# Kernel optimization log

Measured on AMD Instinct MI355X. Metric: run time of the kernel, lower is better.

The kernel has to match this reference:

```python
import jax, jax.numpy as jnp
import numpy as np
from jax.scipy.special import gammaln

N, E, IN, HID, OUT, K, BESSEL_TERMS = 50000, 800000, 64, 64, 32, 10, 20


def setup_inputs() -> dict:
    key = jax.random.key(0)
    ks = jax.random.split(key, 6)
    x = jax.random.normal(ks[0], (N, IN), dtype=jnp.float32)
    edge_index = jax.random.randint(ks[1], (2, E), 0, N, dtype=jnp.int32)
    theta_direct = jax.random.normal(ks[2], (IN, HID), dtype=jnp.float32)
    theta_heat1 = jax.random.normal(ks[3], (IN, HID), dtype=jnp.float32)
    theta_hidden = jax.random.normal(ks[4], (HID, OUT), dtype=jnp.float32)
    theta_heat2 = jax.random.normal(ks[5], (HID, OUT), dtype=jnp.float32)
    t = jnp.array(0.1, dtype=jnp.float32)
    return dict(x=x, edge_index=edge_index, theta_direct=theta_direct,
                theta_heat1=theta_heat1, theta_hidden=theta_hidden,
                theta_heat2=theta_heat2, t=t)


def _bessel_iv(orders, t):
    # Modified Bessel I_v(t) via power series; differentiable in t (t>0, small).
    m = jnp.arange(BESSEL_TERMS, dtype=jnp.float32)  # [M]
    v = orders[:, None]                              # [K,1]
    log_terms = (2.0 * m + v) * jnp.log(t * 0.5) - gammaln(m + 1.0) - gammaln(m + v + 1.0)
    return jnp.exp(log_terms).sum(-1)                # [K]


def _heat_kernel(x, row, col, w, coeffs):
    # Chebyshev recurrence on tilde_L = L_sym - I = -(D^-1/2 A D^-1/2)
    def spmm(v):
        return -jax.ops.segment_sum(w[:, None] * v[col], row, num_segments=N)
    out = coeffs[0] * x
    Tkm2, Tkm1 = x, spmm(x)
    out = out + coeffs[1] * Tkm1
    for k in range(2, K):
        Tk = 2.0 * spmm(Tkm1) - Tkm2
        out = out + coeffs[k] * Tk
        Tkm2, Tkm1 = Tkm1, Tk
    return out


def reference(x, edge_index, theta_direct, theta_heat1, theta_hidden, theta_heat2, t):
    row, col = edge_index[0], edge_index[1]
    # sym-normalized Laplacian edge weights (PyG get_laplacian semantics)
    deg = jax.ops.segment_sum(jnp.ones(E, x.dtype), row, num_segments=N)
    dinv = jnp.where(deg > 0, deg ** -0.5, 0.0)
    w = dinv[row] * dinv[col]                         # [E]
    orders = jnp.arange(K, dtype=jnp.float32)
    iv = _bessel_iv(orders, t)                        # [K]
    signs = jnp.where(orders % 2 == 0, 2.0, -2.0)
    coeffs = (signs * iv).at[0].set(iv[0])            # c0=I0(t), ck=2(-1)^k I_k(t)
    x_heat = _heat_kernel(x, row, col, w, coeffs)
    hidden = jax.nn.relu(x @ theta_direct + x_heat @ theta_heat1)
    hidden_heat = _heat_kernel(hidden, row, col, w, coeffs)
    out = hidden @ theta_hidden + hidden_heat @ theta_heat2
    return jax.nn.log_softmax(out, axis=1)
```

## Files before the change

kernel.cpp:

```cpp
#include <hip/hip_runtime.h>
#include <math.h>

#define N 50000
#define E 800000
#define KCHEB 10
#define BT 20
#define N64 ((size_t)N * 64)
#define UROW ((size_t)(N + 1) * 64)
#define CONV_BLOCKS 1563
#define XU_BLOCKS 1563
#define PAD_BLOCKS 196
#define NB 196
#define EPB 2048
#define ABLK ((E + EPB - 1) / EPB)
#define BCAP 5120
#define PHASE_GRID 1024
#define NGROUP 3125

typedef __attribute__((ext_vector_type(8))) short short8;
typedef __attribute__((ext_vector_type(4))) float f32x4;

__device__ __forceinline__ unsigned f2bf(float x) {
    unsigned u = __float_as_uint(x);
    return (u + 0x7FFFu + ((u >> 16) & 1u)) >> 16;
}
__device__ __forceinline__ float bf2f(unsigned h) {
    return __uint_as_float(h << 16);
}
__device__ __forceinline__ unsigned packbf(float lo, float hi) {
    return f2bf(lo) | (f2bf(hi) << 16);
}
__device__ __forceinline__ void unpack8(uint4 v, float* f) {
    f[0]=bf2f(v.x&0xFFFFu); f[1]=bf2f(v.x>>16);
    f[2]=bf2f(v.y&0xFFFFu); f[3]=bf2f(v.y>>16);
    f[4]=bf2f(v.z&0xFFFFu); f[5]=bf2f(v.z>>16);
    f[6]=bf2f(v.w&0xFFFFu); f[7]=bf2f(v.w>>16);
}
__device__ __forceinline__ uint4 pack8(const float* f) {
    return make_uint4(packbf(f[0],f[1]),packbf(f[2],f[3]),packbf(f[4],f[5]),packbf(f[6],f[7]));
}

__device__ __forceinline__ void pack_one(const float* Wtop, const float* Wbot,
                                         int ncols, uint4* out, int id) {
    int ntiles = ncols >> 4;
    int lane = id & 63;
    int nt = (id >> 6) % ntiles;
    int kt = id / (64 * ntiles);
    int n = nt * 16 + (lane & 15);
    int k0 = kt * 32 + (lane >> 4) * 8;
    const float* src = (k0 < 64) ? (Wtop + k0 * ncols + n) : (Wbot + (k0 - 64) * ncols + n);
    unsigned r[4];
#pragma unroll
    for (int p = 0; p < 4; p++)
        r[p] = packbf(src[(2 * p) * ncols], src[(2 * p + 1) * ncols]);
    out[id] = make_uint4(r[0], r[1], r[2], r[3]);
}

__global__ __launch_bounds__(256) void k1_bucket_conv_pack(
        const int* __restrict__ row, const int* __restrict__ col,
        int* __restrict__ btail, int2* __restrict__ bucketArr,
        const float4* __restrict__ xin, uint4* __restrict__ xbf,
        const float* __restrict__ Wd, const float* __restrict__ Wh1,
        const float* __restrict__ Whd, const float* __restrict__ Wh2,
        uint4* __restrict__ Wfrag1, uint4* __restrict__ Wfrag2) {
    int b = blockIdx.x, tid = threadIdx.x;
    if (b < ABLK) {
        __shared__ int2 buf[EPB];
        __shared__ int cnt[256];
        __shared__ int offs[256];
        __shared__ int gb[256];
        int base = b * EPB;
        int n = E - base; if (n > EPB) n = EPB;
        int r[8], c[8], p[8];
        cnt[tid] = 0;
        __syncthreads();
#pragma unroll
        for (int j = 0; j < 8; j++) {
            int e = base + j * 256 + tid;
            if (e < base + n) {
                r[j] = row[e]; c[j] = col[e];
                p[j] = atomicAdd(&cnt[r[j] >> 8], 1);
            } else r[j] = -1;
        }
        __syncthreads();
        offs[tid] = cnt[tid];
        __syncthreads();
        for (int o = 1; o < 256; o <<= 1) {
            int u = (tid >= o) ? offs[tid - o] : 0;
            __syncthreads();
            offs[tid] += u;
            __syncthreads();
        }
        int excl = offs[tid] - cnt[tid];
        __syncthreads();
        offs[tid] = excl;
        if (tid < NB && cnt[tid] > 0) gb[tid] = atomicAdd(&btail[tid], cnt[tid]);
        __syncthreads();
#pragma unroll
        for (int j = 0; j < 8; j++)
            if (r[j] >= 0) buf[offs[r[j] >> 8] + p[j]] = make_int2(r[j], c[j]);
        __syncthreads();
        for (int i = tid; i < n; i += 256) {
            int2 eg = buf[i];
            int bb = eg.x >> 8;
            int pos = gb[bb] + (i - offs[bb]);
            if (pos < BCAP) bucketArr[(size_t)bb * BCAP + pos] = eg;
        }
    } else if (b < ABLK + CONV_BLOCKS) {
        int i = (b - ABLK) * 256 + tid;
        if (i < (int)(N64 / 8)) {
            float4 a = xin[2 * i], c = xin[2 * i + 1];
            uint4 o;
            o.x = packbf(a.x, a.y); o.y = packbf(a.z, a.w);
            o.z = packbf(c.x, c.y); o.w = packbf(c.z, c.w);
            xbf[i] = o;
        }
    } else if (b < ABLK + CONV_BLOCKS + 4) {
        int id = (b - ABLK - CONV_BLOCKS) * 256 + tid;
        if (id < 1024) pack_one(Wd, Wh1, 64, Wfrag1, id);
    } else {
        int id = (b - ABLK - CONV_BLOCKS - 4) * 256 + tid;
        if (id < 512) pack_one(Whd, Wh2, 32, Wfrag2, id);
    }
}

__global__ __launch_bounds__(256) void k_ell(
        const int2* __restrict__ bucketArr, const int* __restrict__ btail,
        int* __restrict__ ell, int* __restrict__ deg) {
    __shared__ int rcnt[256];
    int b = blockIdx.x, tid = threadIdx.x;
    rcnt[tid] = 0;
    __syncthreads();
    int cnt = btail[b]; if (cnt > BCAP) cnt = BCAP;
    const int2* src = bucketArr + (size_t)b * BCAP;
    for (int i = tid; i < cnt; i += 256) {
        int2 eg = src[i];
        int s = atomicAdd(&rcnt[eg.x & 255], 1);
        if (s < 64) ell[(size_t)eg.x * 64 + s] = eg.y << 7;
    }
    __syncthreads();
    int rr = (b << 8) + tid;
    if (rr < N) deg[rr] = rcnt[tid];
}

__global__ __launch_bounds__(256) void k2_node(
        const float* __restrict__ x, const int* __restrict__ deg,
        float* __restrict__ dinv, unsigned short* __restrict__ xu,
        int* __restrict__ ell, unsigned short* __restrict__ Uarr,
        unsigned short* __restrict__ hidu, int nslots,
        const float* __restrict__ tptr, float* __restrict__ coeffs,
        int* __restrict__ kmaxp) {
    __shared__ float sc[KCHEB];
    int b = blockIdx.x, tid = threadIdx.x;
    if (b < XU_BLOCKS) {
        int i = b * 256 + tid;
        if (i < (int)(N64 / 8)) {
            int r = i >> 3, sub = i & 7;
            int d = deg[r];
            float dr = (d > 0) ? rsqrtf((float)d) : 0.f;
            const float* xp = x + (size_t)r * 64 + sub * 8;
            float4 a = *(const float4*)xp, c = *(const float4*)(xp + 4);
            float f[8] = {dr*a.x, dr*a.y, dr*a.z, dr*a.w, dr*c.x, dr*c.y, dr*c.z, dr*c.w};
            ((uint4*)xu)[i] = pack8(f);
            if (sub == 0) dinv[r] = dr;
        } else if (i < (int)(N64 / 8) + 8) {
            ((uint4*)xu)[i] = make_uint4(0, 0, 0, 0);
        }
    } else if (b < XU_BLOCKS + PAD_BLOCKS) {
        int r = (b - XU_BLOCKS) * 256 + tid;
        if (r < N) {
            int d = deg[r]; if (d > 64) d = 64;
            int dpad = (d + 7) & ~7;
            for (int j = d; j < dpad; j++) ell[(size_t)r * 64 + j] = (N << 7);
        }
    } else if (b == XU_BLOCKS + PAD_BLOCKS) {
        int total = (nslots + 1) * 8;
        if (tid < total) {
            int which = tid >> 3, q = tid & 7;
            uint4* dst = (which < nslots)
                ? (uint4*)(Uarr + (size_t)which * UROW + (size_t)N * 64)
                : (uint4*)(hidu + (size_t)N * 64);
            dst[q] = make_uint4(0, 0, 0, 0);
        }
    } else {
        int v = tid;
        if (v < KCHEB) {
            float tt = tptr[0];
            float lt = logf(0.5f * tt);
            float s = 0.f;
            for (int m = 0; m < BT; m++) {
                float lg = lgammaf((float)m + 1.0f) + lgammaf((float)(m + v) + 1.0f);
                s += expf((2.0f * m + (float)v) * lt - lg);
            }
            float c;
            if (v == 0) c = s;
            else c = ((v & 1) == 0) ? 2.0f * s : -2.0f * s;
            coeffs[v] = c;
            sc[v] = c;
        }
        __syncthreads();
        if (v == 0) {
            float c0 = fabsf(sc[0]);
            int kmax = 1;
            for (int k = 1; k < KCHEB; k++)
                if (fabsf(sc[k]) >= 0.00390625f * c0) kmax = k;
            kmaxp[0] = kmax;
        }
    }
}

__global__ __launch_bounds__(256, 4) void spmm_phase(
        const int* __restrict__ deg, const int* __restrict__ ell,
        const unsigned short* __restrict__ baseu, const unsigned short* __restrict__ baseT,
        unsigned short* __restrict__ Tarr, unsigned short* __restrict__ Uarr,
        int nslots, const float* __restrict__ dinv,
        const int* __restrict__ kmaxp, int* __restrict__ barcnt) {
    int tid = threadIdx.x;
    int lane = tid & 63;
    int lane8 = lane & 7;
    int gbase = lane & 56;
    int h = (lane >> 3) & 1;
    int myoff16 = lane8 * 16;
    int kmax = kmaxp[0]; if (kmax > KCHEB - 1) kmax = KCHEB - 1;
    for (int k = 1; k <= kmax; k++) {
        const unsigned short* uin = (k == 1) ? baseu
                                  : Uarr + (size_t)((k - 2) % nslots) * UROW;
        const uint4* tkm2 = (const uint4*)((k <= 2) ? baseT
                                  : Tarr + (size_t)((k - 3) % nslots) * N64);
        uint4* Tout = (uint4*)(Tarr + (size_t)((k - 1) % nslots) * N64);
        uint4* Uout = (uint4*)(Uarr + (size_t)((k - 1) % nslots) * UROW);
        const char* vbase = (const char*)uin;
        for (int rb = blockIdx.x; rb < NGROUP; rb += PHASE_GRID) {
            int r = rb * 16 + (tid >> 6) * 4 + (lane >> 4);
            int d = deg[r]; if (d > 64) d = 64;
            int dpad = (d + 7) & ~7;
            const int* erow = ell + (size_t)r * 64;
            float a0=0,a1=0,a2=0,a3=0,a4=0,a5=0,a6=0,a7=0;
            for (int j0 = h * 8; j0 < dpad; j0 += 16) {
                int myoff = erow[j0 + lane8];
#pragma unroll
                for (int i = 0; i < 8; i++) {
                    int off = __shfl(myoff, gbase + i, 64);
                    uint4 v = *(const uint4*)(vbase + off + myoff16);
                    a0 += bf2f(v.x & 0xFFFFu);
                    a1 += bf2f(v.x >> 16);
                    a2 += bf2f(v.y & 0xFFFFu);
                    a3 += bf2f(v.y >> 16);
                    a4 += bf2f(v.z & 0xFFFFu);
                    a5 += bf2f(v.z >> 16);
                    a6 += bf2f(v.w & 0xFFFFu);
                    a7 += bf2f(v.w >> 16);
                }
            }
            a0 += __shfl_xor(a0, 8, 64);
            a1 += __shfl_xor(a1, 8, 64);
            a2 += __shfl_xor(a2, 8, 64);
            a3 += __shfl_xor(a3, 8, 64);
            a4 += __shfl_xor(a4, 8, 64);
            a5 += __shfl_xor(a5, 8, 64);
            a6 += __shfl_xor(a6, 8, 64);
            a7 += __shfl_xor(a7, 8, 64);
            if (h == 0) {
                float dr = dinv[r];
                float ndr = -dr;
                float s0=ndr*a0, s1=ndr*a1, s2=ndr*a2, s3=ndr*a3;
                float s4=ndr*a4, s5=ndr*a5, s6=ndr*a6, s7=ndr*a7;
                int idx = r * 8 + lane8;
                if (k >= 2) {
                    uint4 tm = tkm2[idx];
                    s0 = 2.f*s0 - bf2f(tm.x & 0xFFFFu);
                    s1 = 2.f*s1 - bf2f(tm.x >> 16);
                    s2 = 2.f*s2 - bf2f(tm.y & 0xFFFFu);
                    s3 = 2.f*s3 - bf2f(tm.y >> 16);
                    s4 = 2.f*s4 - bf2f(tm.z & 0xFFFFu);
                    s5 = 2.f*s5 - bf2f(tm.z >> 16);
                    s6 = 2.f*s6 - bf2f(tm.w & 0xFFFFu);
                    s7 = 2.f*s7 - bf2f(tm.w >> 16);
                }
                float t8[8] = {s0,s1,s2,s3,s4,s5,s6,s7};
                Tout[idx] = pack8(t8);
                float u8[8] = {dr*s0,dr*s1,dr*s2,dr*s3,dr*s4,dr*s5,dr*s6,dr*s7};
                Uout[idx] = pack8(u8);
            }
        }
        if (k < kmax) {
            __threadfence();
            __syncthreads();
            if (tid == 0) {
                __hip_atomic_fetch_add(barcnt, 1, __ATOMIC_ACQ_REL, __HIP_MEMORY_SCOPE_AGENT);
                int target = PHASE_GRID * k;
                while (__hip_atomic_load(barcnt, __ATOMIC_ACQUIRE, __HIP_MEMORY_SCOPE_AGENT) < target)
                    __builtin_amdgcn_s_sleep(8);
            }
            __syncthreads();
        }
    }
}

__global__ __launch_bounds__(256) void matmul_hidden(
        const unsigned short* __restrict__ basebf, const unsigned short* __restrict__ Tarr,
        int nslots, const float* __restrict__ coeffs, const int* __restrict__ kmaxp,
        const uint4* __restrict__ Wfrag, unsigned short* __restrict__ hidbf,
        const float* __restrict__ dinv, unsigned short* __restrict__ hidu) {
    __shared__ __align__(16) unsigned short At[64][136];
    int tid = threadIdx.x;
    int row0 = blockIdx.x * 64;
    int kmax = kmaxp[0]; if (kmax > KCHEB - 1) kmax = KCHEB - 1;
    float c0 = coeffs[0];
    for (int u = tid; u < 1024; u += 256) {
        int rr = u >> 4, seg = u & 15;
        int r = row0 + rr;
        uint4 val = make_uint4(0, 0, 0, 0);
        int col;
        if (seg < 8) {
            col = seg * 8;
            if (r < N) val = *(const uint4*)(basebf + (size_t)r * 64 + seg * 8);
        } else {
            int s = seg - 8;
            col = 64 + s * 8;
            if (r < N) {
                uint4 xv = *(const uint4*)(basebf + (size_t)r * 64 + s * 8);
                float h[8], f[8];
                unpack8(xv, f);
#pragma unroll
                for (int q = 0; q < 8; q++) h[q] = c0 * f[q];
                for (int j = 1; j <= kmax; j++) {
                    const unsigned short* Tj = Tarr + (size_t)((j - 1) % nslots) * N64;
                    uint4 tv = *(const uint4*)(Tj + (size_t)r * 64 + s * 8);
                    float g[8];
                    unpack8(tv, g);
                    float cj = coeffs[j];
#pragma unroll
                    for (int q = 0; q < 8; q++) h[q] = fmaf(cj, g[q], h[q]);
                }
                val = pack8(h);
            }
        }
        *(uint4*)&At[rr][col] = val;
    }
    __syncthreads();
    int wv = tid >> 6, lane = tid & 63;
    int m0 = wv * 16;
    short8 afr[4];
#pragma unroll
    for (int kt = 0; kt < 4; kt++)
        afr[kt] = *(const short8*)&At[m0 + (lane & 15)][kt * 32 + (lane >> 4) * 8];
    f32x4 acc[4];
#pragma unroll
    for (int nt = 0; nt < 4; nt++) acc[nt] = (f32x4){0.f, 0.f, 0.f, 0.f};
#pragma unroll
    for (int nt = 0; nt < 4; nt++) {
#pragma unroll
        for (int kt = 0; kt < 4; kt++) {
            short8 bfr = *(const short8*)&Wfrag[kt * 256 + nt * 64 + lane];
            acc[nt] = __builtin_amdgcn_mfma_f32_16x16x32_bf16(afr[kt], bfr, acc[nt], 0, 0, 0);
        }
    }
    float drow[4];
#pragma unroll
    for (int i = 0; i < 4; i++) {
        int r = row0 + m0 + (lane >> 4) * 4 + i;
        drow[i] = (r < N) ? dinv[r] : 0.f;
    }
#pragma unroll
    for (int nt = 0; nt < 4; nt++) {
#pragma unroll
        for (int i = 0; i < 4; i++) {
            int r = row0 + m0 + (lane >> 4) * 4 + i;
            if (r < N) {
                float hv = fmaxf(acc[nt][i], 0.f);
                size_t o = (size_t)r * 64 + nt * 16 + (lane & 15);
                hidbf[o] = (unsigned short)f2bf(hv);
                hidu[o]  = (unsigned short)f2bf(drow[i] * hv);
            }
        }
    }
}

__global__ __launch_bounds__(256) void matmul_out(
        const unsigned short* __restrict__ basebf, const unsigned short* __restrict__ Tarr,
        int nslots, const float* __restrict__ coeffs, const int* __restrict__ kmaxp,
        const uint4* __restrict__ Wfrag, float* __restrict__ out) {
    __shared__ __align__(16) unsigned short At[64][136];
    int tid = threadIdx.x;
    int row0 = blockIdx.x * 64;
    int kmax = kmaxp[0]; if (kmax > KCHEB - 1) kmax = KCHEB - 1;
    float c0 = coeffs[0];
    for (int u = tid; u < 1024; u += 256) {
        int rr = u >> 4, seg = u & 15;
        int r = row0 + rr;
        uint4 val = make_uint4(0, 0, 0, 0);
        int col;
        if (seg < 8) {
            col = seg * 8;
            if (r < N) val = *(const uint4*)(basebf + (size_t)r * 64 + seg * 8);
        } else {
            int s = seg - 8;
            col = 64 + s * 8;
            if (r < N) {
                uint4 xv = *(const uint4*)(basebf + (size_t)r * 64 + s * 8);
                float h[8], f[8];
                unpack8(xv, f);
#pragma unroll
                for (int q = 0; q < 8; q++) h[q] = c0 * f[q];
                for (int j = 1; j <= kmax; j++) {
                    const unsigned short* Tj = Tarr + (size_t)((j - 1) % nslots) * N64;
                    uint4 tv = *(const uint4*)(Tj + (size_t)r * 64 + s * 8);
                    float g[8];
                    unpack8(tv, g);
                    float cj = coeffs[j];
#pragma unroll
                    for (int q = 0; q < 8; q++) h[q] = fmaf(cj, g[q], h[q]);
                }
                val = pack8(h);
            }
        }
        *(uint4*)&At[rr][col] = val;
    }
    __syncthreads();
    int wv = tid >> 6, lane = tid & 63;
    int m0 = wv * 16;
    short8 afr[4];
#pragma unroll
    for (int kt = 0; kt < 4; kt++)
        afr[kt] = *(const short8*)&At[m0 + (lane & 15)][kt * 32 + (lane >> 4) * 8];
    f32x4 acc[2];
    acc[0] = (f32x4){0.f, 0.f, 0.f, 0.f};
    acc[1] = (f32x4){0.f, 0.f, 0.f, 0.f};
#pragma unroll
    for (int nt = 0; nt < 2; nt++) {
#pragma unroll
        for (int kt = 0; kt < 4; kt++) {
            short8 bfr = *(const short8*)&Wfrag[kt * 128 + nt * 64 + lane];
            acc[nt] = __builtin_amdgcn_mfma_f32_16x16x32_bf16(afr[kt], bfr, acc[nt], 0, 0, 0);
        }
    }
#pragma unroll
    for (int i = 0; i < 4; i++) {
        float f0 = acc[0][i], f1 = acc[1][i];
        float m = fmaxf(f0, f1);
#pragma unroll
        for (int o = 1; o < 16; o <<= 1) m = fmaxf(m, __shfl_xor(m, o, 64));
        float s = expf(f0 - m) + expf(f1 - m);
#pragma unroll
        for (int o = 1; o < 16; o <<= 1) s += __shfl_xor(s, o, 64);
        float ls = m + logf(s);
        int r = row0 + m0 + (lane >> 4) * 4 + i;
        if (r < N) {
            out[(size_t)r * 32 + (lane & 15)] = f0 - ls;
            out[(size_t)r * 32 + 16 + (lane & 15)] = f1 - ls;
        }
    }
}

extern "C" void kernel_launch(void* const* d_in, const int* in_sizes, int n_in,
                              void* d_out, int out_size, void* d_ws, size_t ws_size,
                              hipStream_t stream) {
    const float* x   = (const float*)d_in[0];
    const int*   ei  = (const int*)d_in[1];
    const float* Wd  = (const float*)d_in[2];
    const float* Wh1 = (const float*)d_in[3];
    const float* Whd = (const float*)d_in[4];
    const float* Wh2 = (const float*)d_in[5];
    const float* tp  = (const float*)d_in[6];
    const int* row = ei;
    const int* col = ei + E;

    size_t off = 0;
    auto alloc = [&](size_t bytes) -> void* {
        void* p = (char*)d_ws + off;
        off += (bytes + 255) & ~(size_t)255;
        return p;
    };
    int*   btail  = (int*)alloc((size_t)512 * 4);
    int*   bar1   = btail + 256;
    int*   bar2   = btail + 257;
    int*   deg    = (int*)alloc((size_t)N * 4);
    float* dinv   = (float*)alloc((size_t)N * 4);
    float* coeffs = (float*)alloc(KCHEB * 4);
    int*   kmaxp  = (int*)alloc(4);
    int*   ell    = (int*)alloc((size_t)N * 64 * 4);
    int2*  bucketArr = (int2*)alloc((size_t)NB * BCAP * 8);
    unsigned short* xbf   = (unsigned short*)alloc(N64 * 2);
    unsigned short* xu    = (unsigned short*)alloc(UROW * 2);
    unsigned short* hidbf = (unsigned short*)alloc(N64 * 2);
    unsigned short* hidu  = (unsigned short*)alloc(UROW * 2);
    uint4* Wfrag1 = (uint4*)alloc(1024 * 16);
    uint4* Wfrag2 = (uint4*)alloc(512 * 16);
    size_t per_slot = N64 * 2 + UROW * 2 + 512;
    int nslots = (int)((ws_size - off) / per_slot);
    if (nslots > KCHEB - 1) nslots = KCHEB - 1;
    if (nslots < 3) nslots = 3;
    unsigned short* Tarr = (unsigned short*)alloc((size_t)nslots * N64 * 2);
    unsigned short* Uarr = (unsigned short*)alloc((size_t)nslots * UROW * 2);

    hipMemsetAsync(btail, 0, (size_t)512 * 4, stream);

    k1_bucket_conv_pack<<<ABLK + CONV_BLOCKS + 6, 256, 0, stream>>>(
        row, col, btail, bucketArr, (const float4*)x, (uint4*)xbf,
        Wd, Wh1, Whd, Wh2, Wfrag1, Wfrag2);
    k_ell<<<NB, 256, 0, stream>>>(bucketArr, btail, ell, deg);
    k2_node<<<XU_BLOCKS + PAD_BLOCKS + 2, 256, 0, stream>>>(
        x, deg, dinv, xu, ell, Uarr, hidu, nslots, tp, coeffs, kmaxp);

    const int mm_grid = (N + 63) / 64;

    spmm_phase<<<PHASE_GRID, 256, 0, stream>>>(deg, ell, xu, xbf,
                                               Tarr, Uarr, nslots, dinv, kmaxp, bar1);
    matmul_hidden<<<mm_grid, 256, 0, stream>>>(xbf, Tarr, nslots, coeffs, kmaxp,
                                               Wfrag1, hidbf, dinv, hidu);

    spmm_phase<<<PHASE_GRID, 256, 0, stream>>>(deg, ell, hidu, hidbf,
                                               Tarr, Uarr, nslots, dinv, kmaxp, bar2);
    matmul_out<<<mm_grid, 256, 0, stream>>>(hidbf, Tarr, nslots, coeffs, kmaxp,
                                            Wfrag2, (float*)d_out);
}
```

Measured before the change: 171.6 us.

## Fuse ELL build with node scaling and raise spmm phase grid and occupancy

Merges the ELL construction kernel and the node preprocessing kernel into one launch. Each bucket block now computes degree, dinv, padding and the dinv-scaled bf16 copy of x for its own 256 rows, and the coefficient block also zeroes the sentinel rows. Separately, the persistent spmm phase grid is doubled and the launch bounds are raised to 8 blocks per CU. The fusion removes one launch and a round trip of deg through memory, but the xu conversion now runs on only 196 blocks. The higher occupancy target may also cause register spills.

Measured after the change: 233.0 us. 1.36x slower.

```diff
diff --git a/kernel.cpp b/kernel.cpp
--- a/kernel.cpp
+++ b/kernel.cpp
@@ -8,13 +8,11 @@
 #define N64 ((size_t)N * 64)
 #define UROW ((size_t)(N + 1) * 64)
 #define CONV_BLOCKS 1563
-#define XU_BLOCKS 1563
-#define PAD_BLOCKS 196
 #define NB 196
 #define EPB 2048
 #define ABLK ((E + EPB - 1) / EPB)
 #define BCAP 5120
-#define PHASE_GRID 1024
+#define PHASE_GRID 2048
 #define NGROUP 3125
 
 typedef __attribute__((ext_vector_type(8))) short short8;
@@ -124,65 +122,55 @@
     }
 }
 
-__global__ __launch_bounds__(256) void k_ell(
+__global__ __launch_bounds__(256) void k_ell_fused(
         const int2* __restrict__ bucketArr, const int* __restrict__ btail,
-        int* __restrict__ ell, int* __restrict__ deg) {
-    __shared__ int rcnt[256];
-    int b = blockIdx.x, tid = threadIdx.x;
-    rcnt[tid] = 0;
-    __syncthreads();
-    int cnt = btail[b]; if (cnt > BCAP) cnt = BCAP;
-    const int2* src = bucketArr + (size_t)b * BCAP;
-    for (int i = tid; i < cnt; i += 256) {
-        int2 eg = src[i];
-        int s = atomicAdd(&rcnt[eg.x & 255], 1);
-        if (s < 64) ell[(size_t)eg.x * 64 + s] = eg.y << 7;
-    }
-    __syncthreads();
-    int rr = (b << 8) + tid;
-    if (rr < N) deg[rr] = rcnt[tid];
-}
-
-__global__ __launch_bounds__(256) void k2_node(
-        const float* __restrict__ x, const int* __restrict__ deg,
-        float* __restrict__ dinv, unsigned short* __restrict__ xu,
-        int* __restrict__ ell, unsigned short* __restrict__ Uarr,
+        int* __restrict__ ell, int* __restrict__ deg,
+        const float* __restrict__ x, float* __restrict__ dinv,
+        unsigned short* __restrict__ xu, unsigned short* __restrict__ Uarr,
         unsigned short* __restrict__ hidu, int nslots,
         const float* __restrict__ tptr, float* __restrict__ coeffs,
         int* __restrict__ kmaxp) {
-    __shared__ float sc[KCHEB];
     int b = blockIdx.x, tid = threadIdx.x;
-    if (b < XU_BLOCKS) {
-        int i = b * 256 + tid;
-        if (i < (int)(N64 / 8)) {
-            int r = i >> 3, sub = i & 7;
-            int d = deg[r];
-            float dr = (d > 0) ? rsqrtf((float)d) : 0.f;
-            const float* xp = x + (size_t)r * 64 + sub * 8;
-            float4 a = *(const float4*)xp, c = *(const float4*)(xp + 4);
-            float f[8] = {dr*a.x, dr*a.y, dr*a.z, dr*a.w, dr*c.x, dr*c.y, dr*c.z, dr*c.w};
-            ((uint4*)xu)[i] = pack8(f);
-            if (sub == 0) dinv[r] = dr;
-        } else if (i < (int)(N64 / 8) + 8) {
-            ((uint4*)xu)[i] = make_uint4(0, 0, 0, 0);
-        }
-    } else if (b < XU_BLOCKS + PAD_BLOCKS) {
-        int r = (b - XU_BLOCKS) * 256 + tid;
-        if (r < N) {
-            int d = deg[r]; if (d > 64) d = 64;
+    if (b < NB) {
+        __shared__ int rcnt[256];
+        __shared__ float sdr[256];
+        rcnt[tid] = 0;
+        __syncthreads();
+        int cnt = btail[b]; if (cnt > BCAP) cnt = BCAP;
+        const int2* src = bucketArr + (size_t)b * BCAP;
+        for (int i = tid; i < cnt; i += 256) {
+            int2 eg = src[i];
+            int s = atomicAdd(&rcnt[eg.x & 255], 1);
+            if (s < 64) ell[(size_t)eg.x * 64 + s] = eg.y << 7;
+        }
+        __syncthreads();
+        int r0 = b << 8;
+        int rr = r0 + tid;
+        int dc = rcnt[tid];
+        int d = dc > 64 ? 64 : dc;
+        float dr = (d > 0) ? rsqrtf((float)d) : 0.f;
+        sdr[tid] = dr;
+        if (rr < N) {
+            deg[rr] = dc;
+            dinv[rr] = dr;
             int dpad = (d + 7) & ~7;
-            for (int j = d; j < dpad; j++) ell[(size_t)r * 64 + j] = (N << 7);
-        }
-    } else if (b == XU_BLOCKS + PAD_BLOCKS) {
-        int total = (nslots + 1) * 8;
-        if (tid < total) {
-            int which = tid >> 3, q = tid & 7;
-            uint4* dst = (which < nslots)
-                ? (uint4*)(Uarr + (size_t)which * UROW + (size_t)N * 64)
-                : (uint4*)(hidu + (size_t)N * 64);
-            dst[q] = make_uint4(0, 0, 0, 0);
+            for (int j = d; j < dpad; j++) ell[(size_t)rr * 64 + j] = (N << 7);
+        }
+        __syncthreads();
+        for (int u = tid; u < 2048; u += 256) {
+            int lr = u >> 3, sub = u & 7;
+            int r = r0 + lr;
+            if (r < N) {
+                float drr = sdr[lr];
+                const float* xp = x + (size_t)r * 64 + sub * 8;
+                float4 a = *(const float4*)xp, c = *(const float4*)(xp + 4);
+                float f[8] = {drr*a.x, drr*a.y, drr*a.z, drr*a.w,
+                              drr*c.x, drr*c.y, drr*c.z, drr*c.w};
+                ((uint4*)xu)[(size_t)r * 8 + sub] = pack8(f);
+            }
         }
     } else {
+        __shared__ float sc[KCHEB];
         int v = tid;
         if (v < KCHEB) {
             float tt = tptr[0];
@@ -206,10 +194,19 @@
                 if (fabsf(sc[k]) >= 0.00390625f * c0) kmax = k;
             kmaxp[0] = kmax;
         }
-    }
-}
-
-__global__ __launch_bounds__(256, 4) void spmm_phase(
+        int total = (nslots + 2) * 8;
+        if (tid < total) {
+            int which = tid >> 3, q = tid & 7;
+            uint4* dst;
+            if (which == 0)           dst = (uint4*)(xu + (size_t)N * 64);
+            else if (which <= nslots) dst = (uint4*)(Uarr + (size_t)(which - 1) * UROW + (size_t)N * 64);
+            else                      dst = (uint4*)(hidu + (size_t)N * 64);
+            dst[q] = make_uint4(0, 0, 0, 0);
+        }
+    }
+}
+
+__global__ __launch_bounds__(256, 8) void spmm_phase(
         const int* __restrict__ deg, const int* __restrict__ ell,
         const unsigned short* __restrict__ baseu, const unsigned short* __restrict__ baseT,
         unsigned short* __restrict__ Tarr, unsigned short* __restrict__ Uarr,
@@ -499,9 +496,8 @@
     k1_bucket_conv_pack<<<ABLK + CONV_BLOCKS + 6, 256, 0, stream>>>(
         row, col, btail, bucketArr, (const float4*)x, (uint4*)xbf,
         Wd, Wh1, Whd, Wh2, Wfrag1, Wfrag2);
-    k_ell<<<NB, 256, 0, stream>>>(bucketArr, btail, ell, deg);
-    k2_node<<<XU_BLOCKS + PAD_BLOCKS + 2, 256, 0, stream>>>(
-        x, deg, dinv, xu, ell, Uarr, hidu, nslots, tp, coeffs, kmaxp);
+    k_ell_fused<<<NB + 1, 256, 0, stream>>>(
+        bucketArr, btail, ell, deg, x, dinv, xu, Uarr, hidu, nslots, tp, coeffs, kmaxp);
 
     const int mm_grid = (N + 63) / 64;
 
```
